# Kernel tuning notes

Measured on AMD Instinct MI355X. Metric: run time of the kernel, lower is better.

The kernel has to match this reference:

```python
import jax, jax.numpy as jnp
import numpy as np


def setup_inputs() -> dict:
    key = jax.random.key(0)
    ks = jax.random.split(key, 6)
    B, S, D, E = 4, 2048, 1024, 8
    H = 4 * D
    return {
        "x": jax.random.normal(ks[0], (B, S, D), dtype=jnp.float32),
        "logits": jax.random.normal(ks[1], (B, S, E), dtype=jnp.float32),
        "noise": jax.random.normal(ks[2], (B, S, E), dtype=jnp.float32),
        "W1": jax.random.normal(ks[3], (E, D, H), dtype=jnp.float32) * (1.0 / np.sqrt(D)),
        "b1": jnp.zeros((E, H), dtype=jnp.float32),
        "W2": jax.random.normal(ks[4], (E, H, D), dtype=jnp.float32) * (1.0 / np.sqrt(H)),
        "b2": jnp.zeros((E, D), dtype=jnp.float32),
        "top_k": 2,
    }


def reference(x, logits, noise, W1, b1, W2, b2, top_k):
    # NoisyTopkRouter_Cluster: noise scaled by softplus(logits), then sparse top-k softmax
    B, S, D = x.shape
    E = logits.shape[-1]
    noisy = logits + noise * jax.nn.softplus(logits)           # [B,S,E]
    _, topi = jax.lax.top_k(noisy, top_k)                      # [B,S,K]
    in_topk = jax.nn.one_hot(topi, E, dtype=jnp.bool_).any(-2)  # [B,S,E]
    sparse = jnp.where(in_topk, noisy, -jnp.inf)
    gates = jax.nn.softmax(sparse, axis=-1)                    # [B,S,E]; zero off top-k

    # SparseMoE combine: sum_e gate[:, e] * Expert_e(x). Gate is exactly 0 for
    # unselected experts, so dense-masked compute matches the gather/scatter loop.
    xf = x.reshape(-1, D)                                      # [T,D]
    gf = gates.reshape(-1, E).T                                # [E,T]

    def body(acc, params):
        w1, bb1, w2, bb2, g = params                           # g: [T]
        h = jax.nn.relu(xf @ w1 + bb1)                         # [T,4D]
        acc = acc + (h @ w2 + bb2) * g[:, None]
        return acc, None

    acc, _ = jax.lax.scan(body, jnp.zeros_like(xf), (W1, b1, W2, b2, gf))
    return acc.reshape(B, S, D)
```

## Files before the change

kernel.cpp:

```cpp
#include <hip/hip_runtime.h>
#include <cstdint>
#include <cstddef>

#define T_TOK 8192
#define E_NUM 8
#define D_DIM 1024
#define H_DIM 4096
#define MAXTILES 136
#define TILE 128
#define BK 32
#define STAGES 3

typedef __attribute__((ext_vector_type(8))) short short8;
typedef __attribute__((ext_vector_type(4))) float f32x4;
typedef __attribute__((ext_vector_type(8))) unsigned short ushort8v;
typedef __attribute__((ext_vector_type(4))) unsigned short ushort4v;

__device__ __forceinline__ unsigned short f2b(float f) {
  unsigned int u = __float_as_uint(f);
  u += 0x7fffu + ((u >> 16) & 1u);
  return (unsigned short)(u >> 16);
}

__device__ __forceinline__ void async16(const void* g, void* l) {
  __builtin_amdgcn_global_load_lds((const __attribute__((address_space(1))) void*)g,
                                   (__attribute__((address_space(3))) void*)l, 16, 0, 0);
}

__global__ void router_kernel(const float* __restrict__ logits, const float* __restrict__ noise,
                              int* __restrict__ counts, int* __restrict__ ti, float* __restrict__ tg) {
  int tk = blockIdx.x * blockDim.x + threadIdx.x;
  if (tk >= T_TOK) return;
  float nz[E_NUM];
#pragma unroll
  for (int e = 0; e < E_NUM; ++e) {
    float l = logits[tk * E_NUM + e];
    float sp = fmaxf(l, 0.f) + log1pf(expf(-fabsf(l)));
    nz[e] = l + noise[tk * E_NUM + e] * sp;
  }
  int i1 = 0; float v1 = nz[0];
#pragma unroll
  for (int e = 1; e < E_NUM; ++e) if (nz[e] > v1) { v1 = nz[e]; i1 = e; }
  int i2 = -1; float v2 = -3.0e38f;
#pragma unroll
  for (int e = 0; e < E_NUM; ++e) if (e != i1 && nz[e] > v2) { v2 = nz[e]; i2 = e; }
  float ex = expf(v2 - v1);
  float g1 = 1.f / (1.f + ex);
  float g2 = ex / (1.f + ex);
  int s1 = atomicAdd(&counts[i1], 1);
  int s2 = atomicAdd(&counts[i2], 1);
  ti[tk*4+0] = i1; ti[tk*4+1] = s1; ti[tk*4+2] = i2; ti[tk*4+3] = s2;
  tg[tk*2+0] = g1; tg[tk*2+1] = g2;
}

__global__ void setup_kernel(const int* __restrict__ counts, int* __restrict__ offs,
                             int* __restrict__ tab) {
  int o = 0;
  for (int e = 0; e < E_NUM; ++e) { offs[e] = o; o += counts[e]; }
  offs[E_NUM] = o;
  int mt = 0;
  for (int e = 0; e < E_NUM; ++e)
    for (int m0 = 0; m0 < counts[e]; m0 += TILE) { tab[mt*2] = e; tab[mt*2+1] = m0; ++mt; }
  for (; mt < MAXTILES; ++mt) { tab[mt*2] = -1; tab[mt*2+1] = 0; }
}

__global__ void gather_kernel(const float* __restrict__ x, const int* __restrict__ ti,
                              const float* __restrict__ tg, const int* __restrict__ offs,
                              unsigned short* __restrict__ xg, int* __restrict__ stok,
                              float* __restrict__ sg) {
  const int tk = blockIdx.x, t = threadIdx.x;
  const int i1 = ti[tk*4+0], s1 = ti[tk*4+1], i2 = ti[tk*4+2], s2 = ti[tk*4+3];
  const int r1 = offs[i1] + s1, r2 = offs[i2] + s2;
  if (t == 0) {
    stok[r1] = tk; sg[r1] = tg[tk*2+0];
    stok[r2] = tk; sg[r2] = tg[tk*2+1];
  }
  const float4 v = *(const float4*)(x + (size_t)tk * D_DIM + t * 4);
  ushort4v bb; bb.x = f2b(v.x); bb.y = f2b(v.y); bb.z = f2b(v.z); bb.w = f2b(v.w);
  *(ushort4v*)(xg + (size_t)r1 * D_DIM + t * 4) = bb;
  *(ushort4v*)(xg + (size_t)r2 * D_DIM + t * 4) = bb;
}

__global__ void transpose_kernel(const float* __restrict__ W, unsigned short* __restrict__ Wt,
                                 int K, int N) {
  const int e = blockIdx.z;
  const float* We = W + (size_t)e * K * N;
  unsigned short* Wte = Wt + (size_t)e * K * N;
  __shared__ __align__(16) unsigned short tb[64 * 72];
  const int n0 = blockIdx.x * 64, k0 = blockIdx.y * 64;
  const int t = threadIdx.x;
  const int kr = t >> 4;
  const int c4 = (t & 15) * 4;
#pragma unroll
  for (int rr = 0; rr < 4; ++rr) {
    int k = kr + rr * 16;
    const float4 v = *(const float4*)(We + (size_t)(k0 + k) * N + n0 + c4);
    tb[(c4+0)*72 + k] = f2b(v.x);
    tb[(c4+1)*72 + k] = f2b(v.y);
    tb[(c4+2)*72 + k] = f2b(v.z);
    tb[(c4+3)*72 + k] = f2b(v.w);
  }
  __syncthreads();
  const int n = t >> 2, kq = (t & 3) * 16;
  ushort8v a = *(const ushort8v*)&tb[n*72 + kq];
  ushort8v b = *(const ushort8v*)&tb[n*72 + kq + 8];
  *(ushort8v*)(Wte + (size_t)(n0+n)*K + k0 + kq) = a;
  *(ushort8v*)(Wte + (size_t)(n0+n)*K + k0 + kq + 8) = b;
}

template<int EPI, int NX>
__global__ __launch_bounds__(256)
void gemm_bt(const unsigned short* __restrict__ A, const unsigned short* __restrict__ Bt,
             const int K, const int N,
             const int* __restrict__ counts, const int* __restrict__ offs,
             const int* __restrict__ tab,
             const float* __restrict__ bias,
             unsigned short* __restrict__ Hout,
             float* __restrict__ Out,
             const int* __restrict__ slot_tok, const float* __restrict__ slot_gate) {
  constexpr int G = NX / 8;
  const int bid = blockIdx.x;
  const int c = bid & 7;
  const int s = bid >> 3;
  const int xi = c * G + (s % G);
  const int mt = s / G;

  const int e = tab[mt*2];
  if (e < 0) return;
  const int m0  = tab[mt*2+1];
  const int cnt = counts[e];
  const int seg = offs[e];
  const int n0  = xi * TILE;

  __shared__ __align__(16) short smem[STAGES * 2 * TILE * BK];
  __shared__ int   s_tok[TILE];
  __shared__ float s_g[TILE];

  const int t = threadIdx.x;
  const int lane = t & 63;
  const int wv = t >> 6;
  const int wm = wv & 1, wn = wv >> 1;
  const int fr = lane & 15, fq = lane >> 4;

  if (EPI == 1 && t < TILE) {
    int rl = m0 + t;
    if (rl < cnt) { s_tok[t] = slot_tok[seg + rl]; s_g[t] = slot_gate[seg + rl]; }
    else          { s_tok[t] = 0;                  s_g[t] = 0.f; }
  }
  __syncthreads();

  const unsigned short* Ae = A + (size_t)seg * K;
  const unsigned short* Be = Bt + (size_t)e * N * K + (size_t)n0 * K;

  const int row0 = t >> 2;
  const int kcg  = (((t & 3) - (t >> 3)) & 3) * 8;
  int ar0 = m0 + row0;        ar0 = ar0 < cnt ? ar0 : cnt - 1;
  int ar1 = m0 + row0 + 64;   ar1 = ar1 < cnt ? ar1 : cnt - 1;
  const unsigned short* rA0 = Ae + (size_t)ar0 * K + kcg;
  const unsigned short* rA1 = Ae + (size_t)ar1 * K + kcg;
  const unsigned short* rB0 = Be + (size_t)row0 * K + kcg;
  const unsigned short* rB1 = Be + (size_t)(row0 + 64) * K + kcg;
  const int ldsOff = wv * 1024;

  auto issue = [&](int koff, int soff) {
    char* pA = (char*)smem + soff + ldsOff;
    char* pB = (char*)smem + soff + 8192 + ldsOff;
    async16(rA0 + koff, pA);
    async16(rA1 + koff, pA + 4096);
    async16(rB0 + koff, pB);
    async16(rB1 + koff, pB + 4096);
  };

  f32x4 acc[4][4];
#pragma unroll
  for (int i = 0; i < 4; ++i)
#pragma unroll
    for (int j = 0; j < 4; ++j) acc[i][j] = (f32x4){0.f, 0.f, 0.f, 0.f};

  issue(0 * BK, 0 * 16384);
  issue(1 * BK, 1 * 16384);
  issue(2 * BK, 2 * 16384);

  const int csw = ((fq + (fr >> 1)) & 3) * 8;

  int soff = 0;
  for (int k0 = 0; k0 < K; k0 += BK) {
    asm volatile("s_waitcnt vmcnt(8)" ::: "memory");
    asm volatile("s_barrier" ::: "memory");

    const short* As = (const short*)((const char*)smem + soff);
    const short* Bs = (const short*)((const char*)smem + soff + 8192);
    short8 af[4], bf[4];
#pragma unroll
    for (int i = 0; i < 4; ++i) {
      int row = wm*64 + i*16 + fr;
      af[i] = *(const short8*)&As[row*BK + csw];
    }
#pragma unroll
    for (int j = 0; j < 4; ++j) {
      int row = wn*64 + j*16 + fr;
      bf[j] = *(const short8*)&Bs[row*BK + csw];
    }
#pragma unroll
    for (int i = 0; i < 4; ++i)
#pragma unroll
      for (int j = 0; j < 4; ++j)
        acc[i][j] = __builtin_amdgcn_mfma_f32_16x16x32_bf16(af[i], bf[j], acc[i][j], 0, 0, 0);

    asm volatile("s_barrier" ::: "memory");

    int kpre = k0 + STAGES * BK;
    if (kpre > K - BK) kpre = K - BK;
    issue(kpre, soff);
    soff += 16384; if (soff == STAGES * 16384) soff = 0;
  }

  if (EPI == 0) {
    const float* be = bias + (size_t)e * N;
#pragma unroll
    for (int j = 0; j < 4; ++j) {
      int col = n0 + wn*64 + j*16 + fr;
      float bv = be[col];
#pragma unroll
      for (int i = 0; i < 4; ++i) {
        int rb = m0 + wm*64 + i*16 + fq*4;
#pragma unroll
        for (int r = 0; r < 4; ++r) {
          int rl = rb + r;
          if (rl < cnt) {
            float v = acc[i][j][r] + bv;
            v = v > 0.f ? v : 0.f;
            Hout[(size_t)(seg + rl) * N + col] = f2b(v);
          }
        }
      }
    }
  } else {
    const float* be = bias + (size_t)e * N;
#pragma unroll
    for (int j = 0; j < 4; ++j) {
      int col = n0 + wn*64 + j*16 + fr;
      float bv = be[col];
#pragma unroll
      for (int i = 0; i < 4; ++i) {
        int rbt = wm*64 + i*16 + fq*4;
#pragma unroll
        for (int r = 0; r < 4; ++r) {
          int rlt = rbt + r;
          if (m0 + rlt < cnt) {
            float v = (acc[i][j][r] + bv) * s_g[rlt];
            unsafeAtomicAdd(Out + (size_t)s_tok[rlt] * N + col, v);
          }
        }
      }
    }
  }
}

extern "C" void kernel_launch(void* const* d_in, const int* in_sizes, int n_in,
                              void* d_out, int out_size, void* d_ws, size_t ws_size,
                              hipStream_t stream) {
  const float* x      = (const float*)d_in[0];
  const float* logits = (const float*)d_in[1];
  const float* noise  = (const float*)d_in[2];
  const float* W1     = (const float*)d_in[3];
  const float* b1     = (const float*)d_in[4];
  const float* W2     = (const float*)d_in[5];
  const float* b2     = (const float*)d_in[6];
  float* out = (float*)d_out;

  char* ws = (char*)d_ws;
  size_t off = 0;
  auto alloc = [&](size_t b) { size_t o = off; off = (off + b + 255) & ~(size_t)255; return o; };
  size_t o_counts = alloc(E_NUM * 4);
  size_t o_offs   = alloc((E_NUM + 1) * 4);
  size_t o_tab    = alloc((size_t)MAXTILES * 2 * 4);
  size_t o_ti     = alloc((size_t)T_TOK * 4 * 4);
  size_t o_tg     = alloc((size_t)T_TOK * 2 * 4);
  size_t o_stok   = alloc((size_t)2 * T_TOK * 4);
  size_t o_sg     = alloc((size_t)2 * T_TOK * 4);
  size_t o_xg     = alloc((size_t)2 * T_TOK * D_DIM * 2);
  size_t o_w1t    = alloc((size_t)E_NUM * D_DIM * H_DIM * 2);
  size_t o_w2t    = alloc((size_t)E_NUM * D_DIM * H_DIM * 2);
  size_t o_h      = alloc((size_t)2 * T_TOK * H_DIM * 2);
  if (off > ws_size) return;

  int*            counts = (int*)(ws + o_counts);
  int*            offsp  = (int*)(ws + o_offs);
  int*            tab    = (int*)(ws + o_tab);
  int*            ti     = (int*)(ws + o_ti);
  float*          tg     = (float*)(ws + o_tg);
  int*            stok   = (int*)(ws + o_stok);
  float*          sg     = (float*)(ws + o_sg);
  unsigned short* xg     = (unsigned short*)(ws + o_xg);
  unsigned short* w1t    = (unsigned short*)(ws + o_w1t);
  unsigned short* w2t    = (unsigned short*)(ws + o_w2t);
  unsigned short* h      = (unsigned short*)(ws + o_h);

  hipMemsetAsync(out, 0, (size_t)out_size * sizeof(float), stream);
  hipMemsetAsync(counts, 0, E_NUM * sizeof(int), stream);

  router_kernel<<<T_TOK / 256, 256, 0, stream>>>(logits, noise, counts, ti, tg);
  setup_kernel<<<1, 1, 0, stream>>>(counts, offsp, tab);
  gather_kernel<<<T_TOK, 256, 0, stream>>>(x, ti, tg, offsp, xg, stok, sg);

  transpose_kernel<<<dim3(H_DIM/64, D_DIM/64, E_NUM), 256, 0, stream>>>(W1, w1t, D_DIM, H_DIM);
  transpose_kernel<<<dim3(D_DIM/64, H_DIM/64, E_NUM), 256, 0, stream>>>(W2, w2t, H_DIM, D_DIM);

  gemm_bt<0, H_DIM/TILE><<<dim3((H_DIM/TILE) * MAXTILES), 256, 0, stream>>>(
      xg, w1t, D_DIM, H_DIM, counts, offsp, tab, b1, h, nullptr, nullptr, nullptr);
  gemm_bt<1, D_DIM/TILE><<<dim3((D_DIM/TILE) * MAXTILES), 256, 0, stream>>>(
      h, w2t, H_DIM, D_DIM, counts, offsp, tab, b2, nullptr, out, stok, sg);
}
```

Before: 930.6 us.

## Enlarge GEMM tiles to 256 with 512 threads and split-K the second GEMM

Doubles the GEMM tile to 256x256 with 8 waves per block, each wave computing 128x64, to raise data reuse per LDS load. The second GEMM gets a 4-way split-K, with partial sums combined by the existing atomic adds and the bias added only by the first split. This keeps enough blocks for the smaller N=1024 GEMM. The block-index swizzle is rewritten to map blocks to XCDs linearly. The cost is more LDS (96KB of staging buffers), higher register pressure, and four times as many atomics on the output.

```diff
diff --git a/kernel.cpp b/kernel.cpp
--- a/kernel.cpp
+++ b/kernel.cpp
@@ -6,8 +6,8 @@
 #define E_NUM 8
 #define D_DIM 1024
 #define H_DIM 4096
-#define MAXTILES 136
-#define TILE 128
+#define MAXTILES 72
+#define TILE 256
 #define BK 32
 #define STAGES 3
 
@@ -108,8 +108,8 @@
   *(ushort8v*)(Wte + (size_t)(n0+n)*K + k0 + kq + 8) = b;
 }
 
-template<int EPI, int NX>
-__global__ __launch_bounds__(256)
+template<int EPI, int NX, int KSPLIT>
+__global__ __launch_bounds__(512, 2)
 void gemm_bt(const unsigned short* __restrict__ A, const unsigned short* __restrict__ Bt,
              const int K, const int N,
              const int* __restrict__ counts, const int* __restrict__ offs,
@@ -118,12 +118,14 @@
              unsigned short* __restrict__ Hout,
              float* __restrict__ Out,
              const int* __restrict__ slot_tok, const float* __restrict__ slot_gate) {
-  constexpr int G = NX / 8;
+  constexpr int GRID = NX * MAXTILES * KSPLIT;
+  constexpr int Q = GRID / 8;
   const int bid = blockIdx.x;
-  const int c = bid & 7;
-  const int s = bid >> 3;
-  const int xi = c * G + (s % G);
-  const int mt = s / G;
+  const int lin = (bid & 7) * Q + (bid >> 3);
+  const int mt  = lin % MAXTILES;
+  const int u   = lin / MAXTILES;
+  const int kb  = u % KSPLIT;
+  const int xi  = u / KSPLIT;
 
   const int e = tab[mt*2];
   if (e < 0) return;
@@ -131,6 +133,9 @@
   const int cnt = counts[e];
   const int seg = offs[e];
   const int n0  = xi * TILE;
+  const int KC  = K / KSPLIT;
+  const int ks  = kb * KC;
+  const int kend = ks + KC;
 
   __shared__ __align__(16) short smem[STAGES * 2 * TILE * BK];
   __shared__ int   s_tok[TILE];
@@ -139,7 +144,7 @@
   const int t = threadIdx.x;
   const int lane = t & 63;
   const int wv = t >> 6;
-  const int wm = wv & 1, wn = wv >> 1;
+  const int wm = wv >> 2, wn = wv & 3;
   const int fr = lane & 15, fq = lane >> 4;
 
   if (EPI == 1 && t < TILE) {
@@ -152,67 +157,62 @@
   const unsigned short* Ae = A + (size_t)seg * K;
   const unsigned short* Be = Bt + (size_t)e * N * K + (size_t)n0 * K;
 
-  const int row0 = t >> 2;
-  const int kcg  = (((t & 3) - (t >> 3)) & 3) * 8;
-  int ar0 = m0 + row0;        ar0 = ar0 < cnt ? ar0 : cnt - 1;
-  int ar1 = m0 + row0 + 64;   ar1 = ar1 < cnt ? ar1 : cnt - 1;
-  const unsigned short* rA0 = Ae + (size_t)ar0 * K + kcg;
-  const unsigned short* rA1 = Ae + (size_t)ar1 * K + kcg;
-  const unsigned short* rB0 = Be + (size_t)row0 * K + kcg;
-  const unsigned short* rB1 = Be + (size_t)(row0 + 64) * K + kcg;
-  const int ldsOff = wv * 1024;
-
-  auto issue = [&](int koff, int soff) {
-    char* pA = (char*)smem + soff + ldsOff;
-    char* pB = (char*)smem + soff + 8192 + ldsOff;
-    async16(rA0 + koff, pA);
-    async16(rA1 + koff, pA + 4096);
-    async16(rB0 + koff, pB);
-    async16(rB1 + koff, pB + 4096);
+  const int rt = t >> 2;
+  const int kc = (((t & 3) - (t >> 3)) & 3) * 8;
+  int ar0 = m0 + rt;         ar0 = ar0 < cnt ? ar0 : cnt - 1;
+  int ar1 = m0 + 128 + rt;   ar1 = ar1 < cnt ? ar1 : cnt - 1;
+  const unsigned short* rA0 = Ae + (size_t)ar0 * K + kc;
+  const unsigned short* rA1 = Ae + (size_t)ar1 * K + kc;
+  const unsigned short* rB0 = Be + (size_t)rt * K + kc;
+  const unsigned short* rB1 = Be + (size_t)(128 + rt) * K + kc;
+  const int ldsW = wv * 1024;
+
+  auto issue = [&](int ksh, int soff) {
+    char* pA = (char*)smem + soff + ldsW;
+    char* pB = (char*)smem + soff + 16384 + ldsW;
+    async16(rA0 + ksh, pA);
+    async16(rA1 + ksh, pA + 8192);
+    async16(rB0 + ksh, pB);
+    async16(rB1 + ksh, pB + 8192);
   };
 
-  f32x4 acc[4][4];
-#pragma unroll
-  for (int i = 0; i < 4; ++i)
+  f32x4 acc[8][4];
+#pragma unroll
+  for (int i = 0; i < 8; ++i)
 #pragma unroll
     for (int j = 0; j < 4; ++j) acc[i][j] = (f32x4){0.f, 0.f, 0.f, 0.f};
 
-  issue(0 * BK, 0 * 16384);
-  issue(1 * BK, 1 * 16384);
-  issue(2 * BK, 2 * 16384);
+  issue(ks + 0 * BK, 0 * 32768);
+  issue(ks + 1 * BK, 1 * 32768);
+  issue(ks + 2 * BK, 2 * 32768);
 
   const int csw = ((fq + (fr >> 1)) & 3) * 8;
 
   int soff = 0;
-  for (int k0 = 0; k0 < K; k0 += BK) {
+  for (int k0 = ks; k0 < kend; k0 += BK) {
     asm volatile("s_waitcnt vmcnt(8)" ::: "memory");
     asm volatile("s_barrier" ::: "memory");
 
     const short* As = (const short*)((const char*)smem + soff);
-    const short* Bs = (const short*)((const char*)smem + soff + 8192);
-    short8 af[4], bf[4];
-#pragma unroll
-    for (int i = 0; i < 4; ++i) {
-      int row = wm*64 + i*16 + fr;
-      af[i] = *(const short8*)&As[row*BK + csw];
+    const short* Bs = (const short*)((const char*)smem + soff + 16384);
+    short8 bfv[4];
+#pragma unroll
+    for (int j = 0; j < 4; ++j)
+      bfv[j] = *(const short8*)&Bs[(wn*64 + j*16 + fr)*BK + csw];
+#pragma unroll
+    for (int i = 0; i < 8; ++i) {
+      short8 af = *(const short8*)&As[(wm*128 + i*16 + fr)*BK + csw];
+#pragma unroll
+      for (int j = 0; j < 4; ++j)
+        acc[i][j] = __builtin_amdgcn_mfma_f32_16x16x32_bf16(af, bfv[j], acc[i][j], 0, 0, 0);
     }
-#pragma unroll
-    for (int j = 0; j < 4; ++j) {
-      int row = wn*64 + j*16 + fr;
-      bf[j] = *(const short8*)&Bs[row*BK + csw];
-    }
-#pragma unroll
-    for (int i = 0; i < 4; ++i)
-#pragma unroll
-      for (int j = 0; j < 4; ++j)
-        acc[i][j] = __builtin_amdgcn_mfma_f32_16x16x32_bf16(af[i], bf[j], acc[i][j], 0, 0, 0);
 
     asm volatile("s_barrier" ::: "memory");
 
     int kpre = k0 + STAGES * BK;
-    if (kpre > K - BK) kpre = K - BK;
+    if (kpre > kend - BK) kpre = kend - BK;
     issue(kpre, soff);
-    soff += 16384; if (soff == STAGES * 16384) soff = 0;
+    soff += 32768; if (soff == STAGES * 32768) soff = 0;
   }
 
   if (EPI == 0) {
@@ -222,15 +222,15 @@
       int col = n0 + wn*64 + j*16 + fr;
       float bv = be[col];
 #pragma unroll
-      for (int i = 0; i < 4; ++i) {
-        int rb = m0 + wm*64 + i*16 + fq*4;
+      for (int i = 0; i < 8; ++i) {
+        int tl0 = wm*128 + i*16 + fq*4;
 #pragma unroll
         for (int r = 0; r < 4; ++r) {
-          int rl = rb + r;
-          if (rl < cnt) {
+          int tlr = tl0 + r;
+          if (m0 + tlr < cnt) {
             float v = acc[i][j][r] + bv;
             v = v > 0.f ? v : 0.f;
-            Hout[(size_t)(seg + rl) * N + col] = f2b(v);
+            Hout[(size_t)(seg + m0 + tlr) * N + col] = f2b(v);
           }
         }
       }
@@ -240,16 +240,16 @@
 #pragma unroll
     for (int j = 0; j < 4; ++j) {
       int col = n0 + wn*64 + j*16 + fr;
-      float bv = be[col];
-#pragma unroll
-      for (int i = 0; i < 4; ++i) {
-        int rbt = wm*64 + i*16 + fq*4;
+      float bv = (kb == 0) ? be[col] : 0.f;
+#pragma unroll
+      for (int i = 0; i < 8; ++i) {
+        int tl0 = wm*128 + i*16 + fq*4;
 #pragma unroll
         for (int r = 0; r < 4; ++r) {
-          int rlt = rbt + r;
-          if (m0 + rlt < cnt) {
-            float v = (acc[i][j][r] + bv) * s_g[rlt];
-            unsafeAtomicAdd(Out + (size_t)s_tok[rlt] * N + col, v);
+          int tlr = tl0 + r;
+          if (m0 + tlr < cnt) {
+            float v = (acc[i][j][r] + bv) * s_g[tlr];
+            unsafeAtomicAdd(Out + (size_t)s_tok[tlr] * N + col, v);
           }
         }
       }
@@ -307,8 +307,8 @@
   transpose_kernel<<<dim3(H_DIM/64, D_DIM/64, E_NUM), 256, 0, stream>>>(W1, w1t, D_DIM, H_DIM);
   transpose_kernel<<<dim3(D_DIM/64, H_DIM/64, E_NUM), 256, 0, stream>>>(W2, w2t, H_DIM, D_DIM);
 
-  gemm_bt<0, H_DIM/TILE><<<dim3((H_DIM/TILE) * MAXTILES), 256, 0, stream>>>(
+  gemm_bt<0, H_DIM/TILE, 1><<<dim3((H_DIM/TILE) * MAXTILES * 1), 512, 0, stream>>>(
       xg, w1t, D_DIM, H_DIM, counts, offsp, tab, b1, h, nullptr, nullptr, nullptr);
-  gemm_bt<1, D_DIM/TILE><<<dim3((D_DIM/TILE) * MAXTILES), 256, 0, stream>>>(
+  gemm_bt<1, D_DIM/TILE, 4><<<dim3((D_DIM/TILE) * MAXTILES * 4), 512, 0, stream>>>(
       h, w2t, H_DIM, D_DIM, counts, offsp, tab, b2, nullptr, out, stok, sg);
 }
```

After: 1.085 ms. +16.6%, slower.
